# Performance work log

Measured on AMD Instinct MI355X. Metric: run time of the kernel, lower is better.

Reference implementation:

```python
import jax, jax.numpy as jnp
import numpy as np

B, M, H, D, K, V = 32, 4096, 32, 4096, 128, 128

def setup_inputs() -> dict:
    key = jax.random.key(0)
    ks = jax.random.split(key, 7)
    s = lambda fan: 1.0 / np.sqrt(fan)
    return {
        "x": jax.random.normal(ks[0], (B, D), jnp.float32),
        "K_prev": jax.random.normal(ks[1], (B, M, K), jnp.float32),
        "V_prev": jax.random.normal(ks[2], (B, M, V), jnp.float32),
        "P_q": jax.random.normal(ks[3], (H, D, K), jnp.float32) * s(D),
        "P_k": jax.random.normal(ks[4], (D, K), jnp.float32) * s(D),
        "P_v": jax.random.normal(ks[5], (D, V), jnp.float32) * s(D),
        "P_o": jax.random.normal(ks[6], (H, D, V), jnp.float32) * s(D),
    }

def reference(x, K_prev, V_prev, P_q, P_k, P_v, P_o):
    # per-head query projection: [b,d] x [h,d,k] -> [b,h,k]
    q = jnp.einsum('bd,hdk->bhk', x, P_q)
    # shared (multi-query) K/V projection of the new token, appended to cache
    k_new = jnp.einsum('bd,dk->bk', x, P_k)          # [b,k]
    v_new = jnp.einsum('bd,dv->bv', x, P_v)          # [b,v]
    K_new = jnp.concatenate([K_prev, k_new[:, None, :]], axis=1)  # [b,m+1,k]
    V_new = jnp.concatenate([V_prev, v_new[:, None, :]], axis=1)  # [b,m+1,v]
    # attention over shared cache
    logits = jnp.einsum('bhk,bmk->bhm', q, K_new)    # [b,h,m+1]
    w = jax.nn.softmax(logits, axis=-1)
    o = jnp.einsum('bhm,bmv->bhv', w, V_new)         # [b,h,v]
    y = jnp.einsum('bhv,hdv->bd', o, P_o)            # [b,d]
    return (y, K_new, V_new)
```

## Files before the change

kernel.cpp:

```cpp
#include <hip/hip_runtime.h>

#define B_ 32
#define M_ 4096
#define M1_ 4097
#define H_ 32
#define D_ 4096

typedef float float4_ __attribute__((ext_vector_type(4)));
typedef float f32x4 __attribute__((ext_vector_type(4)));
typedef short short8 __attribute__((ext_vector_type(8)));
typedef short short4_ __attribute__((ext_vector_type(4)));

#define KOFF 131072
#define VOFF 16912384

#define Q_OFF     0u
#define O_OFF     139264u
#define YPART_OFF 270336u
#define QPART_OFF 1318912u
#define APO_OFF   1318912u
#define MSUM_OFF  2433024u

#define WAITV(n) asm volatile("s_waitcnt vmcnt(" #n ")" ::: "memory")
#define SBAR() __builtin_amdgcn_sched_barrier(0)

__device__ __forceinline__ unsigned short f2bf(float f) {
  union { float f; unsigned u; } cv; cv.f = f;
  return (unsigned short)((cv.u + 0x7FFFu + ((cv.u >> 16) & 1u)) >> 16);
}
__device__ __forceinline__ float bf2f(unsigned short b) {
  union { unsigned u; float f; } cv; cv.u = ((unsigned)b) << 16;
  return cv.f;
}
__device__ __forceinline__ short8 pack8(const float* t) {
  short8 r;
#pragma unroll
  for (int j = 0; j < 8; ++j) r[j] = (short)f2bf(t[j]);
  return r;
}
__device__ __forceinline__ short8 load8cvt(const float* __restrict__ p) {
  float t[8];
  float4_ v0 = *(const float4_*)p;
  float4_ v1 = *(const float4_*)(p + 4);
#pragma unroll
  for (int j = 0; j < 4; ++j) { t[j] = v0[j]; t[4 + j] = v1[j]; }
  return pack8(t);
}
__device__ __forceinline__ float4_ ntld4(const float* p) {
  return __builtin_nontemporal_load((const float4_*)p);
}
__device__ __forceinline__ float ntldf(const float* p) {
  return __builtin_nontemporal_load(p);
}
__device__ __forceinline__ void ntst4(float* p, float4_ v) {
  __builtin_nontemporal_store(v, (float4_*)p);
}
__device__ __forceinline__ short8 load8cvt_nt(const float* __restrict__ p) {
  float t[8];
  float4_ v0 = ntld4(p);
  float4_ v1 = ntld4(p + 4);
#pragma unroll
  for (int j = 0; j < 4; ++j) { t[j] = v0[j]; t[4 + j] = v1[j]; }
  return pack8(t);
}
__device__ __forceinline__ void load_lds16(const float* g, float* l) {
  __builtin_amdgcn_global_load_lds(
      (const __attribute__((address_space(1))) unsigned int*)g,
      (__attribute__((address_space(3))) unsigned int*)l, 16, 0, 0);
}

__global__ __launch_bounds__(256) void k_proj(const float* __restrict__ x,
    const float* __restrict__ Pq, const float* __restrict__ Pk,
    const float* __restrict__ Pv, unsigned short* __restrict__ qpart)
{
  int bid = blockIdx.x;
  int hh = bid >> 4;
  int c  = bid & 15;
  const float* W = (hh < 32) ? (Pq + (size_t)hh * D_ * 128)
                             : ((hh == 32) ? Pk : Pv);
  int d0 = c * 256;
  int tid = threadIdx.x;
  int w = tid >> 6, l = tid & 63, l15 = l & 15, lg = l >> 4;
  f32x4 acc[2][2] = {};
  for (int ks = 0; ks < 8; ++ks) {
    int dk = d0 + ks * 32 + lg * 8;
    short8 af[2];
#pragma unroll
    for (int bt = 0; bt < 2; ++bt)
      af[bt] = load8cvt(x + (size_t)(bt * 16 + l15) * D_ + dk);
    short8 bf[2];
#pragma unroll
    for (int nti = 0; nti < 2; ++nti) {
      int col = (2 * w + nti) * 16 + l15;
      float t[8];
#pragma unroll
      for (int j = 0; j < 8; ++j) t[j] = ntldf(&W[(size_t)(dk + j) * 128 + col]);
      bf[nti] = pack8(t);
    }
#pragma unroll
    for (int bt = 0; bt < 2; ++bt)
#pragma unroll
      for (int nti = 0; nti < 2; ++nti)
        acc[bt][nti] = __builtin_amdgcn_mfma_f32_16x16x32_bf16(af[bt], bf[nti], acc[bt][nti], 0, 0, 0);
  }
#pragma unroll
  for (int bt = 0; bt < 2; ++bt)
#pragma unroll
    for (int nti = 0; nti < 2; ++nti) {
      int k = (2 * w + nti) * 16 + l15;
#pragma unroll
      for (int i = 0; i < 4; ++i) {
        int b = bt * 16 + lg * 4 + i;
        __builtin_nontemporal_store(f2bf(acc[bt][nti][i]),
            &qpart[(size_t)((c * 34 + hh) * 32 + b) * 128 + k]);
      }
    }
}

__global__ __launch_bounds__(256) void k_reduce_q(const unsigned short* __restrict__ qpart,
    float* __restrict__ q, float* __restrict__ dout)
{
  int idx = blockIdx.x * 256 + threadIdx.x;
  if (idx >= 34 * 32 * 128) return;
  float s = 0.f;
#pragma unroll
  for (int cc = 0; cc < 16; ++cc)
    s += bf2f(__builtin_nontemporal_load(&qpart[(size_t)cc * 139264 + idx]));
  q[idx] = s;
  int hh = idx >> 12;
  if (hh >= 32) {
    int b = (idx >> 7) & 31, k = idx & 127;
    size_t off = (hh == 32) ? (size_t)KOFF : (size_t)VOFF;
    __builtin_nontemporal_store(s, &dout[off + ((size_t)b * M1_ + M_) * 128 + k]);
  }
}

#define ISSUE(T, KR, VB) do { \
  const float* Kc_ = Kb + (T) * 16 * 128; \
  const float* Vc_ = Vb + (T) * 16 * 128; \
  const float* Krow_ = Kc_ + (size_t)l15 * 128; \
  _Pragma("unroll") \
  for (int ks = 0; ks < 4; ++ks) { \
    KR[2 * ks]     = ntld4(Krow_ + ks * 32 + lg * 8); \
    KR[2 * ks + 1] = ntld4(Krow_ + ks * 32 + lg * 8 + 4); \
  } \
  _Pragma("unroll") \
  for (int i = 0; i < 8; ++i) load_lds16(Vc_ + i * 256 + l * 4, VB + i * 256); \
} while (0)

#define DO_CHUNK(T, KR, VB) do { \
   \
  float* Knrow_ = Knb + (T) * 16 * 128 + (size_t)l15 * 128; \
  _Pragma("unroll") \
  for (int ks = 0; ks < 4; ++ks) { \
    ntst4(Knrow_ + ks * 32 + lg * 8,     KR[2 * ks]); \
    ntst4(Knrow_ + ks * 32 + lg * 8 + 4, KR[2 * ks + 1]); \
  } \
   \
  float* Vnc_ = Vnb + (T) * 16 * 128; \
  _Pragma("unroll") \
  for (int i = 0; i < 8; ++i) { \
    float4_ t_ = *(const float4_*)(VB + (i * 64 + l) * 4); \
    ntst4(Vnc_ + (size_t)(i * 64 + l) * 4, t_); \
  } \
   \
  short8 kf_[4]; \
  _Pragma("unroll") \
  for (int ks = 0; ks < 4; ++ks) { \
    float tt_[8]; \
    _Pragma("unroll") \
    for (int j = 0; j < 4; ++j) { tt_[j] = KR[2 * ks][j]; tt_[4 + j] = KR[2 * ks + 1][j]; } \
    kf_[ks] = pack8(tt_); \
  } \
   \
  f32x4 sacc_[2] = {}; \
  _Pragma("unroll") \
  for (int ks = 0; ks < 4; ++ks) \
    _Pragma("unroll") \
    for (int ht = 0; ht < 2; ++ht) \
      sacc_[ht] = __builtin_amdgcn_mfma_f32_16x16x32_bf16(af[ht][ks], kf_[ks], sacc_[ht], 0, 0, 0); \
   \
  _Pragma("unroll") \
  for (int ht = 0; ht < 2; ++ht) { \
    f32x4 mx_; \
    _Pragma("unroll") \
    for (int i = 0; i < 4; ++i) { \
      float v_ = sacc_[ht][i]; \
      v_ = fmaxf(v_, __shfl_xor(v_, 1)); v_ = fmaxf(v_, __shfl_xor(v_, 2)); \
      v_ = fmaxf(v_, __shfl_xor(v_, 4)); v_ = fmaxf(v_, __shfl_xor(v_, 8)); \
      mx_[i] = v_; \
    } \
    f32x4 fsc_; \
    _Pragma("unroll") \
    for (int i = 0; i < 4; ++i) { \
      float mn_ = fmaxf(mrun[ht][i], mx_[i]); \
      fsc_[i] = __expf(mrun[ht][i] - mn_); \
      mrun[ht][i] = mn_; \
    } \
    _Pragma("unroll") \
    for (int vt = 0; vt < 8; ++vt) oacc[ht][vt] *= fsc_; \
    _Pragma("unroll") \
    for (int i = 0; i < 4; ++i) { \
      float p_ = __expf(sacc_[ht][i] - mrun[ht][i]); \
      lsum[ht][i] = lsum[ht][i] * fsc_[i] + p_; \
      Plds[w][ht * 16 + lg * 4 + i][l15] = f2bf(p_); \
    } \
  } \
  asm volatile("" ::: "memory"); \
   \
  short8 z_ = {}; \
  short8 pa_[2]; \
  _Pragma("unroll") \
  for (int ht = 0; ht < 2; ++ht) \
    pa_[ht] = (lg < 2) ? *(const short8*)&Plds[w][ht * 16 + l15][lg * 8] : z_; \
  _Pragma("unroll") \
  for (int vt = 0; vt < 8; ++vt) { \
    short8 bfv_ = z_; \
    if (lg < 2) { \
      float t_[8]; \
      _Pragma("unroll") \
      for (int j = 0; j < 8; ++j) t_[j] = VB[(lg * 8 + j) * 128 + vt * 16 + l15]; \
      bfv_ = pack8(t_); \
    } \
    _Pragma("unroll") \
    for (int ht = 0; ht < 2; ++ht) \
      oacc[ht][vt] = __builtin_amdgcn_mfma_f32_16x16x32_bf16(pa_[ht], bfv_, oacc[ht][vt], 0, 0, 0); \
  } \
} while (0)

__global__ __launch_bounds__(256, 2) void k_attn(const float* __restrict__ Kp,
    const float* __restrict__ Vp, const float* __restrict__ q,
    float* __restrict__ dout, unsigned short* __restrict__ apo,
    float* __restrict__ msum)
{
  __shared__ float Vbuf[4][2][2048];
  __shared__ unsigned short Plds[4][32][16];
  __shared__ float Mh[4][32], Sh[4][32];
  int bid = blockIdx.x;
  int b = bid >> 4;
  int tid = threadIdx.x, w = tid >> 6, l = tid & 63, l15 = l & 15, lg = l >> 4;
  int wid = (bid & 15) * 4 + w;
  const float* Kb = Kp + ((size_t)b * M_ + wid * 64) * 128;
  const float* Vb = Vp + ((size_t)b * M_ + wid * 64) * 128;
  float* Knb = dout + KOFF + ((size_t)b * M1_ + wid * 64) * 128;
  float* Vnb = dout + VOFF + ((size_t)b * M1_ + wid * 64) * 128;
  float* vb0 = &Vbuf[w][0][0];
  float* vb1 = &Vbuf[w][1][0];

  short8 af[2][4];
#pragma unroll
  for (int ks = 0; ks < 4; ++ks)
#pragma unroll
    for (int ht = 0; ht < 2; ++ht)
      af[ht][ks] = load8cvt(q + (size_t)((ht * 16 + l15) * 32 + b) * 128 + ks * 32 + lg * 8);

  float4_ krA[8], krB[8];
  f32x4 mrun[2], lsum[2], oacc[2][8];
#pragma unroll
  for (int ht = 0; ht < 2; ++ht) {
#pragma unroll
    for (int i = 0; i < 4; ++i) { mrun[ht][i] = -3e38f; lsum[ht][i] = 0.f; }
#pragma unroll
    for (int vt = 0; vt < 8; ++vt) oacc[ht][vt] = f32x4{0.f, 0.f, 0.f, 0.f};
  }

  ISSUE(0, krA, vb0); SBAR();
  ISSUE(1, krB, vb1); SBAR();
  WAITV(16); SBAR();
  DO_CHUNK(0, krA, vb0);
  ISSUE(2, krA, vb0); SBAR();
  WAITV(32); SBAR();
  DO_CHUNK(1, krB, vb1);
  ISSUE(3, krB, vb1); SBAR();
  WAITV(32); SBAR();
  DO_CHUNK(2, krA, vb0);
  WAITV(16); SBAR();
  DO_CHUNK(3, krB, vb1);

#pragma unroll
  for (int ht = 0; ht < 2; ++ht)
#pragma unroll
    for (int i = 0; i < 4; ++i) {
      float s = lsum[ht][i];
      s += __shfl_xor(s, 1); s += __shfl_xor(s, 2);
      s += __shfl_xor(s, 4); s += __shfl_xor(s, 8);
      lsum[ht][i] = s;
    }
  if (l15 == 0) {
#pragma unroll
    for (int ht = 0; ht < 2; ++ht)
#pragma unroll
      for (int i = 0; i < 4; ++i) {
        int h = ht * 16 + lg * 4 + i;
        Mh[w][h] = mrun[ht][i];
        Sh[w][h] = lsum[ht][i];
      }
  }
  __syncthreads();
  float* Ob = &Vbuf[w][0][0];
#pragma unroll
  for (int ht = 0; ht < 2; ++ht)
#pragma unroll
    for (int i = 0; i < 4; ++i) {
      int h = ht * 16 + lg * 4 + i;
      float ms = fmaxf(fmaxf(Mh[0][h], Mh[1][h]), fmaxf(Mh[2][h], Mh[3][h]));
      float f = __expf(mrun[ht][i] - ms);
#pragma unroll
      for (int vt = 0; vt < 8; ++vt)
        Ob[h * 128 + vt * 16 + l15] = oacc[ht][vt][i] * f;
    }
  __syncthreads();
  int blk = bid & 15;
  size_t sblk = ((size_t)b * 16 + blk) * 32;
  if (tid < 32) {
    int h = tid;
    float ms = fmaxf(fmaxf(Mh[0][h], Mh[1][h]), fmaxf(Mh[2][h], Mh[3][h]));
    float ss = Sh[0][h] * __expf(Mh[0][h] - ms) + Sh[1][h] * __expf(Mh[1][h] - ms)
             + Sh[2][h] * __expf(Mh[2][h] - ms) + Sh[3][h] * __expf(Mh[3][h] - ms);
    msum[(sblk + h) * 2]     = ms;
    msum[(sblk + h) * 2 + 1] = ss;
  }
  const float* Vall = &Vbuf[0][0][0];
  for (int idx = tid; idx < 4096; idx += 256) {
    float s = Vall[idx] + Vall[4096 + idx] + Vall[8192 + idx] + Vall[12288 + idx];
    __builtin_nontemporal_store(f2bf(s), &apo[(sblk + (idx >> 7)) * 128 + (idx & 127)]);
  }
}

__global__ __launch_bounds__(256) void k_combine(const unsigned short* __restrict__ apo,
    const float* __restrict__ msum, const float* __restrict__ q, float* __restrict__ o)
{
  __shared__ float redN[4][128];
  __shared__ float redD[4];
  int bid = blockIdx.x;
  int b = bid >> 5, h = bid & 31;
  int tid = threadIdx.x, w = tid >> 6, l = tid & 63;

  const float* qh = q + (size_t)(h * 32 + b) * 128;
  const float* kn = q + (size_t)(1024 + b) * 128;
  const float* vn = q + (size_t)(1056 + b) * 128;
  float e = qh[2 * l] * kn[2 * l] + qh[2 * l + 1] * kn[2 * l + 1];
#pragma unroll
  for (int d = 1; d < 64; d <<= 1) e += __shfl_xor(e, d);

  float gm = (l < 16) ? msum[((size_t)(b * 16 + l) * 32 + h) * 2] : -3e38f;
#pragma unroll
  for (int d = 1; d < 64; d <<= 1) gm = fmaxf(gm, __shfl_xor(gm, d));
  gm = fmaxf(gm, e);
  float pe = __expf(e - gm);

  float num0 = 0.f, num1 = 0.f, den = 0.f;
#pragma unroll
  for (int i = 0; i < 4; ++i) {
    int cc = w * 4 + i;
    size_t slot = (size_t)(b * 16 + cc) * 32 + h;
    float sc = __expf(msum[slot * 2] - gm);
    den += sc * msum[slot * 2 + 1];
    unsigned pp = __builtin_nontemporal_load((const unsigned*)&apo[slot * 128 + l * 2]);
    num0 += sc * bf2f((unsigned short)(pp & 0xFFFFu));
    num1 += sc * bf2f((unsigned short)(pp >> 16));
  }
  redN[w][l * 2] = num0;
  redN[w][l * 2 + 1] = num1;
  if (l == 0) redD[w] = den + (w == 0 ? pe : 0.f);
  __syncthreads();
  if (tid < 128) {
    float num = redN[0][tid] + redN[1][tid] + redN[2][tid] + redN[3][tid] + pe * vn[tid];
    float dd  = redD[0] + redD[1] + redD[2] + redD[3];
    o[((size_t)(b * 32 + h)) * 128 + tid] = num / dd;
  }
}

__global__ __launch_bounds__(256) void k_out(const float* __restrict__ o,
    const float* __restrict__ Po, float* __restrict__ ypart)
{
  int bid = blockIdx.x;
  int dt = bid >> 3, hg = bid & 7;
  int tid = threadIdx.x, w = tid >> 6, l = tid & 63, l15 = l & 15, lg = l >> 4;
  int d = dt * 64 + w * 16 + l15;
  f32x4 acc[2] = {};
  for (int hi = 0; hi < 4; ++hi) {
    int h = hg * 4 + hi;
#pragma unroll
    for (int ks = 0; ks < 4; ++ks) {
      short8 af[2];
#pragma unroll
      for (int bt = 0; bt < 2; ++bt)
        af[bt] = load8cvt(o + ((size_t)((bt * 16 + l15) * 32 + h)) * 128 + ks * 32 + lg * 8);
      short8 bf = load8cvt_nt(Po + ((size_t)h * D_ + d) * 128 + ks * 32 + lg * 8);
#pragma unroll
      for (int bt = 0; bt < 2; ++bt)
        acc[bt] = __builtin_amdgcn_mfma_f32_16x16x32_bf16(af[bt], bf, acc[bt], 0, 0, 0);
    }
  }
#pragma unroll
  for (int bt = 0; bt < 2; ++bt)
#pragma unroll
    for (int i = 0; i < 4; ++i) {
      int b = bt * 16 + lg * 4 + i;
      __builtin_nontemporal_store(acc[bt][i],
          &ypart[((size_t)(hg * 32 + b)) * 4096 + d]);
    }
}

__global__ __launch_bounds__(256) void k_reduce_y(const float* __restrict__ ypart,
    float* __restrict__ dout)
{
  int idx = blockIdx.x * 256 + threadIdx.x;
  float s = 0.f;
#pragma unroll
  for (int g = 0; g < 8; ++g)
    s += __builtin_nontemporal_load(&ypart[(size_t)g * 131072 + idx]);
  dout[idx] = s;
}

extern "C" void kernel_launch(void* const* d_in, const int* in_sizes, int n_in,
                              void* d_out, int out_size, void* d_ws, size_t ws_size,
                              hipStream_t stream) {
  (void)in_sizes; (void)n_in; (void)out_size; (void)ws_size;
  const float* x  = (const float*)d_in[0];
  const float* Kp = (const float*)d_in[1];
  const float* Vp = (const float*)d_in[2];
  const float* Pq = (const float*)d_in[3];
  const float* Pk = (const float*)d_in[4];
  const float* Pv = (const float*)d_in[5];
  const float* Po = (const float*)d_in[6];
  float* out = (float*)d_out;
  float* ws  = (float*)d_ws;
  float* q     = ws + Q_OFF;
  float* o     = ws + O_OFF;
  float* ypart = ws + YPART_OFF;
  unsigned short* qpart = (unsigned short*)(ws + QPART_OFF);
  unsigned short* apo   = (unsigned short*)(ws + APO_OFF);
  float* msum  = ws + MSUM_OFF;

  hipLaunchKernelGGL(k_proj,     dim3(544),  dim3(256), 0, stream, x, Pq, Pk, Pv, qpart);
  hipLaunchKernelGGL(k_reduce_q, dim3(544),  dim3(256), 0, stream, qpart, q, out);
  hipLaunchKernelGGL(k_attn,     dim3(512),  dim3(256), 0, stream, Kp, Vp, q, out, apo, msum);
  hipLaunchKernelGGL(k_combine,  dim3(1024), dim3(256), 0, stream, apo, msum, q, o);
  hipLaunchKernelGGL(k_out,      dim3(512),  dim3(256), 0, stream, o, Po, ypart);
  hipLaunchKernelGGL(k_reduce_y, dim3(512),  dim3(256), 0, stream, ypart, out);
}
```

Measured before the change: 126.3 us.

## Copy K cache via coalesced row loads, separate from MFMA fragment loads

Each K chunk is now read twice. One read uses a contiguous per-lane layout and feeds the K_new copy, so the global stores are fully coalesced. A second read in the per-row fragment layout feeds the bf16 MFMA. Nontemporal load and store hints are swapped for plain accesses, and the wait-count schedule for the two-buffer pipeline is reworked. This gives better-coalesced write traffic in exchange for extra K read requests, which may hit L2, and more registers per lane. It also gives up the cache-bypass hints on a streaming copy.

```diff
diff --git a/kernel.cpp b/kernel.cpp
--- a/kernel.cpp
+++ b/kernel.cpp
@@ -51,9 +51,6 @@
 }
 __device__ __forceinline__ float ntldf(const float* p) {
   return __builtin_nontemporal_load(p);
-}
-__device__ __forceinline__ void ntst4(float* p, float4_ v) {
-  __builtin_nontemporal_store(v, (float4_*)p);
 }
 __device__ __forceinline__ short8 load8cvt_nt(const float* __restrict__ p) {
   float t[8];
@@ -135,33 +132,34 @@
   }
 }
 
-#define ISSUE(T, KR, VB) do { \
-  const float* Kc_ = Kb + (T) * 16 * 128; \
-  const float* Vc_ = Vb + (T) * 16 * 128; \
+#define ISSUE(T, KRC, KRF, VB) do { \
+  const float* Kc_ = Kb + (T) * 2048; \
+   \
+  _Pragma("unroll") \
+  for (int i = 0; i < 8; ++i) KRC[i] = *(const float4_*)(Kc_ + (i * 64 + l) * 4); \
+   \
   const float* Krow_ = Kc_ + (size_t)l15 * 128; \
   _Pragma("unroll") \
   for (int ks = 0; ks < 4; ++ks) { \
-    KR[2 * ks]     = ntld4(Krow_ + ks * 32 + lg * 8); \
-    KR[2 * ks + 1] = ntld4(Krow_ + ks * 32 + lg * 8 + 4); \
+    KRF[2 * ks]     = *(const float4_*)(Krow_ + ks * 32 + lg * 8); \
+    KRF[2 * ks + 1] = *(const float4_*)(Krow_ + ks * 32 + lg * 8 + 4); \
   } \
+  const float* Vc_ = Vb + (T) * 2048; \
   _Pragma("unroll") \
   for (int i = 0; i < 8; ++i) load_lds16(Vc_ + i * 256 + l * 4, VB + i * 256); \
 } while (0)
 
-#define DO_CHUNK(T, KR, VB) do { \
-   \
-  float* Knrow_ = Knb + (T) * 16 * 128 + (size_t)l15 * 128; \
-  _Pragma("unroll") \
-  for (int ks = 0; ks < 4; ++ks) { \
-    ntst4(Knrow_ + ks * 32 + lg * 8,     KR[2 * ks]); \
-    ntst4(Knrow_ + ks * 32 + lg * 8 + 4, KR[2 * ks + 1]); \
-  } \
-   \
-  float* Vnc_ = Vnb + (T) * 16 * 128; \
+#define DO_CHUNK(T, KRC, KRF, VB) do { \
+   \
+  float* Knc_ = Knb + (T) * 2048; \
+  _Pragma("unroll") \
+  for (int i = 0; i < 8; ++i) *(float4_*)(Knc_ + (size_t)(i * 64 + l) * 4) = KRC[i]; \
+   \
+  float* Vnc_ = Vnb + (T) * 2048; \
   _Pragma("unroll") \
   for (int i = 0; i < 8; ++i) { \
     float4_ t_ = *(const float4_*)(VB + (i * 64 + l) * 4); \
-    ntst4(Vnc_ + (size_t)(i * 64 + l) * 4, t_); \
+    *(float4_*)(Vnc_ + (size_t)(i * 64 + l) * 4) = t_; \
   } \
    \
   short8 kf_[4]; \
@@ -169,7 +167,7 @@
   for (int ks = 0; ks < 4; ++ks) { \
     float tt_[8]; \
     _Pragma("unroll") \
-    for (int j = 0; j < 4; ++j) { tt_[j] = KR[2 * ks][j]; tt_[4 + j] = KR[2 * ks + 1][j]; } \
+    for (int j = 0; j < 4; ++j) { tt_[j] = KRF[2 * ks][j]; tt_[4 + j] = KRF[2 * ks + 1][j]; } \
     kf_[ks] = pack8(tt_); \
   } \
    \
@@ -254,7 +252,7 @@
     for (int ht = 0; ht < 2; ++ht)
       af[ht][ks] = load8cvt(q + (size_t)((ht * 16 + l15) * 32 + b) * 128 + ks * 32 + lg * 8);
 
-  float4_ krA[8], krB[8];
+  float4_ krA[8], krB[8], kfrA[8], kfrB[8];
   f32x4 mrun[2], lsum[2], oacc[2][8];
 #pragma unroll
   for (int ht = 0; ht < 2; ++ht) {
@@ -264,18 +262,19 @@
     for (int vt = 0; vt < 8; ++vt) oacc[ht][vt] = f32x4{0.f, 0.f, 0.f, 0.f};
   }
 
-  ISSUE(0, krA, vb0); SBAR();
-  ISSUE(1, krB, vb1); SBAR();
+  ISSUE(0, krA, kfrA, vb0); SBAR();
+  WAITV(24); SBAR();
+  ISSUE(1, krB, kfrB, vb1); SBAR();
+  WAITV(24); SBAR();
+  DO_CHUNK(0, krA, kfrA, vb0);
   WAITV(16); SBAR();
-  DO_CHUNK(0, krA, vb0);
-  ISSUE(2, krA, vb0); SBAR();
-  WAITV(32); SBAR();
-  DO_CHUNK(1, krB, vb1);
-  ISSUE(3, krB, vb1); SBAR();
-  WAITV(32); SBAR();
-  DO_CHUNK(2, krA, vb0);
+  ISSUE(2, krA, kfrA, vb0); SBAR();
+  DO_CHUNK(1, krB, kfrB, vb1);
   WAITV(16); SBAR();
-  DO_CHUNK(3, krB, vb1);
+  ISSUE(3, krB, kfrB, vb1); SBAR();
+  DO_CHUNK(2, krA, kfrA, vb0);
+  WAITV(16); SBAR();
+  DO_CHUNK(3, krB, kfrB, vb1);
 
 #pragma unroll
   for (int ht = 0; ht < 2; ++ht)
```

Measured after the change: 139.7 us. +10.7%, slower.

## Split KV cache copy into a separate kernel ahead of attention

Applied to the files above, without the earlier changes.

Moves copying K_prev/V_prev into the output cache out of the attention kernel into a dedicated streaming copy kernel. The attention kernel then only reads K/V with regular (cacheable) loads, and its wait counts are adjusted for the removed stores. The aim is to shorten the attention inner loop and rely on the last-level cache holding K/V after the copy. The risk is that K/V are read from memory twice if they are not cache resident, and an extra launch is added.

```diff
diff --git a/kernel.cpp b/kernel.cpp
--- a/kernel.cpp
+++ b/kernel.cpp
@@ -51,9 +51,6 @@
 }
 __device__ __forceinline__ float ntldf(const float* p) {
   return __builtin_nontemporal_load(p);
-}
-__device__ __forceinline__ void ntst4(float* p, float4_ v) {
-  __builtin_nontemporal_store(v, (float4_*)p);
 }
 __device__ __forceinline__ short8 load8cvt_nt(const float* __restrict__ p) {
   float t[8];
@@ -135,34 +132,39 @@
   }
 }
 
+__global__ __launch_bounds__(256) void k_copy(const float* __restrict__ Kp,
+    const float* __restrict__ Vp, float* __restrict__ dout)
+{
+  int bid = blockIdx.x;
+  int arr = bid >> 11;
+  int blk = bid & 2047;
+  const float4_* src = (const float4_*)(arr ? Vp : Kp);
+  float* dstbase = dout + (arr ? VOFF : KOFF);
+  size_t f0 = (size_t)blk * 2048;
+  size_t b = f0 >> 17;
+  size_t r0 = f0 & 131071;
+  float* dst = dstbase + b * ((size_t)M1_ * 128);
+  float4_ t[8];
+#pragma unroll
+  for (int i = 0; i < 8; ++i) t[i] = src[f0 + i * 256 + threadIdx.x];
+#pragma unroll
+  for (int i = 0; i < 8; ++i)
+    __builtin_nontemporal_store(t[i], (float4_*)(dst + (r0 + i * 256 + threadIdx.x) * 4));
+}
+
 #define ISSUE(T, KR, VB) do { \
-  const float* Kc_ = Kb + (T) * 16 * 128; \
-  const float* Vc_ = Vb + (T) * 16 * 128; \
-  const float* Krow_ = Kc_ + (size_t)l15 * 128; \
+  const float* Krow_ = Kb + (T) * 2048 + (size_t)l15 * 128; \
   _Pragma("unroll") \
   for (int ks = 0; ks < 4; ++ks) { \
-    KR[2 * ks]     = ntld4(Krow_ + ks * 32 + lg * 8); \
-    KR[2 * ks + 1] = ntld4(Krow_ + ks * 32 + lg * 8 + 4); \
+    KR[2 * ks]     = *(const float4_*)(Krow_ + ks * 32 + lg * 8); \
+    KR[2 * ks + 1] = *(const float4_*)(Krow_ + ks * 32 + lg * 8 + 4); \
   } \
+  const float* Vc_ = Vb + (T) * 2048; \
   _Pragma("unroll") \
   for (int i = 0; i < 8; ++i) load_lds16(Vc_ + i * 256 + l * 4, VB + i * 256); \
 } while (0)
 
 #define DO_CHUNK(T, KR, VB) do { \
-   \
-  float* Knrow_ = Knb + (T) * 16 * 128 + (size_t)l15 * 128; \
-  _Pragma("unroll") \
-  for (int ks = 0; ks < 4; ++ks) { \
-    ntst4(Knrow_ + ks * 32 + lg * 8,     KR[2 * ks]); \
-    ntst4(Knrow_ + ks * 32 + lg * 8 + 4, KR[2 * ks + 1]); \
-  } \
-   \
-  float* Vnc_ = Vnb + (T) * 16 * 128; \
-  _Pragma("unroll") \
-  for (int i = 0; i < 8; ++i) { \
-    float4_ t_ = *(const float4_*)(VB + (i * 64 + l) * 4); \
-    ntst4(Vnc_ + (size_t)(i * 64 + l) * 4, t_); \
-  } \
    \
   short8 kf_[4]; \
   _Pragma("unroll") \
@@ -230,8 +232,7 @@
 
 __global__ __launch_bounds__(256, 2) void k_attn(const float* __restrict__ Kp,
     const float* __restrict__ Vp, const float* __restrict__ q,
-    float* __restrict__ dout, unsigned short* __restrict__ apo,
-    float* __restrict__ msum)
+    unsigned short* __restrict__ apo, float* __restrict__ msum)
 {
   __shared__ float Vbuf[4][2][2048];
   __shared__ unsigned short Plds[4][32][16];
@@ -242,8 +243,6 @@
   int wid = (bid & 15) * 4 + w;
   const float* Kb = Kp + ((size_t)b * M_ + wid * 64) * 128;
   const float* Vb = Vp + ((size_t)b * M_ + wid * 64) * 128;
-  float* Knb = dout + KOFF + ((size_t)b * M1_ + wid * 64) * 128;
-  float* Vnb = dout + VOFF + ((size_t)b * M1_ + wid * 64) * 128;
   float* vb0 = &Vbuf[w][0][0];
   float* vb1 = &Vbuf[w][1][0];
 
@@ -269,12 +268,12 @@
   WAITV(16); SBAR();
   DO_CHUNK(0, krA, vb0);
   ISSUE(2, krA, vb0); SBAR();
-  WAITV(32); SBAR();
+  WAITV(16); SBAR();
   DO_CHUNK(1, krB, vb1);
   ISSUE(3, krB, vb1); SBAR();
-  WAITV(32); SBAR();
+  WAITV(16); SBAR();
   DO_CHUNK(2, krA, vb0);
-  WAITV(16); SBAR();
+  WAITV(0); SBAR();
   DO_CHUNK(3, krB, vb1);
 
 #pragma unroll
@@ -436,7 +435,8 @@
 
   hipLaunchKernelGGL(k_proj,     dim3(544),  dim3(256), 0, stream, x, Pq, Pk, Pv, qpart);
   hipLaunchKernelGGL(k_reduce_q, dim3(544),  dim3(256), 0, stream, qpart, q, out);
-  hipLaunchKernelGGL(k_attn,     dim3(512),  dim3(256), 0, stream, Kp, Vp, q, out, apo, msum);
+  hipLaunchKernelGGL(k_copy,     dim3(4096), dim3(256), 0, stream, Kp, Vp, out);
+  hipLaunchKernelGGL(k_attn,     dim3(512),  dim3(256), 0, stream, Kp, Vp, q, apo, msum);
   hipLaunchKernelGGL(k_combine,  dim3(1024), dim3(256), 0, stream, apo, msum, q, o);
   hipLaunchKernelGGL(k_out,      dim3(512),  dim3(256), 0, stream, o, Po, ypart);
   hipLaunchKernelGGL(k_reduce_y, dim3(512),  dim3(256), 0, stream, ypart, out);
```

Result: slower. 135.8 us (+7.5%).

## Stage projection weights through double-buffered LDS and store y partials as bf16

Applied to the files above, without the earlier changes.

In k_proj the weight matrix used to be read with strided scalar non-temporal loads, one column element per row. It is now loaded as coalesced float4 rows, converted to bf16, and written into a double-buffered LDS tile, with the next k-slice prefetched while the current one is consumed. This adds a __syncthreads per slice and sets launch bounds to 4 blocks. Separately, the y partial sums from k_out are stored as bf16 rather than fp32, halving the write and read traffic of the reduction, at some cost in output precision.

```diff
diff --git a/kernel.cpp b/kernel.cpp
--- a/kernel.cpp
+++ b/kernel.cpp
@@ -49,12 +49,6 @@
 __device__ __forceinline__ float4_ ntld4(const float* p) {
   return __builtin_nontemporal_load((const float4_*)p);
 }
-__device__ __forceinline__ float ntldf(const float* p) {
-  return __builtin_nontemporal_load(p);
-}
-__device__ __forceinline__ void ntst4(float* p, float4_ v) {
-  __builtin_nontemporal_store(v, (float4_*)p);
-}
 __device__ __forceinline__ short8 load8cvt_nt(const float* __restrict__ p) {
   float t[8];
   float4_ v0 = ntld4(p);
@@ -69,10 +63,11 @@
       (__attribute__((address_space(3))) unsigned int*)l, 16, 0, 0);
 }
 
-__global__ __launch_bounds__(256) void k_proj(const float* __restrict__ x,
+__global__ __launch_bounds__(256, 4) void k_proj(const float* __restrict__ x,
     const float* __restrict__ Pq, const float* __restrict__ Pk,
     const float* __restrict__ Pv, unsigned short* __restrict__ qpart)
 {
+  __shared__ unsigned short Wl[2][32][128];
   int bid = blockIdx.x;
   int hh = bid >> 4;
   int c  = bid & 15;
@@ -81,8 +76,27 @@
   int d0 = c * 256;
   int tid = threadIdx.x;
   int w = tid >> 6, l = tid & 63, l15 = l & 15, lg = l >> 4;
+  int sdr = tid >> 5, sk4 = (tid & 31) * 4;
   f32x4 acc[2][2] = {};
+  float4_ tmp[4];
+#pragma unroll
+  for (int i = 0; i < 4; ++i)
+    tmp[i] = ntld4(W + (size_t)(d0 + i * 8 + sdr) * 128 + sk4);
   for (int ks = 0; ks < 8; ++ks) {
+    int buf = ks & 1;
+#pragma unroll
+    for (int i = 0; i < 4; ++i) {
+      short4_ s;
+#pragma unroll
+      for (int j = 0; j < 4; ++j) s[j] = (short)f2bf(tmp[i][j]);
+      *(short4_*)&Wl[buf][i * 8 + sdr][sk4] = s;
+    }
+    if (ks < 7) {
+#pragma unroll
+      for (int i = 0; i < 4; ++i)
+        tmp[i] = ntld4(W + (size_t)(d0 + (ks + 1) * 32 + i * 8 + sdr) * 128 + sk4);
+    }
+    __syncthreads();
     int dk = d0 + ks * 32 + lg * 8;
     short8 af[2];
 #pragma unroll
@@ -92,10 +106,10 @@
 #pragma unroll
     for (int nti = 0; nti < 2; ++nti) {
       int col = (2 * w + nti) * 16 + l15;
-      float t[8];
-#pragma unroll
-      for (int j = 0; j < 8; ++j) t[j] = ntldf(&W[(size_t)(dk + j) * 128 + col]);
-      bf[nti] = pack8(t);
+      short8 t;
+#pragma unroll
+      for (int j = 0; j < 8; ++j) t[j] = (short)Wl[buf][lg * 8 + j][col];
+      bf[nti] = t;
     }
 #pragma unroll
     for (int bt = 0; bt < 2; ++bt)
@@ -153,15 +167,15 @@
   float* Knrow_ = Knb + (T) * 16 * 128 + (size_t)l15 * 128; \
   _Pragma("unroll") \
   for (int ks = 0; ks < 4; ++ks) { \
-    ntst4(Knrow_ + ks * 32 + lg * 8,     KR[2 * ks]); \
-    ntst4(Knrow_ + ks * 32 + lg * 8 + 4, KR[2 * ks + 1]); \
+    __builtin_nontemporal_store(KR[2 * ks],     (float4_*)(Knrow_ + ks * 32 + lg * 8)); \
+    __builtin_nontemporal_store(KR[2 * ks + 1], (float4_*)(Knrow_ + ks * 32 + lg * 8 + 4)); \
   } \
    \
   float* Vnc_ = Vnb + (T) * 16 * 128; \
   _Pragma("unroll") \
   for (int i = 0; i < 8; ++i) { \
     float4_ t_ = *(const float4_*)(VB + (i * 64 + l) * 4); \
-    ntst4(Vnc_ + (size_t)(i * 64 + l) * 4, t_); \
+    __builtin_nontemporal_store(t_, (float4_*)(Vnc_ + (size_t)(i * 64 + l) * 4)); \
   } \
    \
   short8 kf_[4]; \
@@ -372,7 +386,7 @@
 }
 
 __global__ __launch_bounds__(256) void k_out(const float* __restrict__ o,
-    const float* __restrict__ Po, float* __restrict__ ypart)
+    const float* __restrict__ Po, unsigned short* __restrict__ ypart)
 {
   int bid = blockIdx.x;
   int dt = bid >> 3, hg = bid & 7;
@@ -398,19 +412,19 @@
 #pragma unroll
     for (int i = 0; i < 4; ++i) {
       int b = bt * 16 + lg * 4 + i;
-      __builtin_nontemporal_store(acc[bt][i],
+      __builtin_nontemporal_store(f2bf(acc[bt][i]),
           &ypart[((size_t)(hg * 32 + b)) * 4096 + d]);
     }
 }
 
-__global__ __launch_bounds__(256) void k_reduce_y(const float* __restrict__ ypart,
+__global__ __launch_bounds__(256) void k_reduce_y(const unsigned short* __restrict__ ypart,
     float* __restrict__ dout)
 {
   int idx = blockIdx.x * 256 + threadIdx.x;
   float s = 0.f;
 #pragma unroll
   for (int g = 0; g < 8; ++g)
-    s += __builtin_nontemporal_load(&ypart[(size_t)g * 131072 + idx]);
+    s += bf2f(__builtin_nontemporal_load(&ypart[(size_t)g * 131072 + idx]));
   dout[idx] = s;
 }
 
@@ -429,7 +443,7 @@
   float* ws  = (float*)d_ws;
   float* q     = ws + Q_OFF;
   float* o     = ws + O_OFF;
-  float* ypart = ws + YPART_OFF;
+  unsigned short* ypart = (unsigned short*)(ws + YPART_OFF);
   unsigned short* qpart = (unsigned short*)(ws + QPART_OFF);
   unsigned short* apo   = (unsigned short*)(ws + APO_OFF);
   float* msum  = ws + MSUM_OFF;
```

Measured after the change: 124.6 us (median of 2 runs). Within noise of the previous version (-1.3%).
